# Kernel tuning notes

Hardware: AMD Instinct MI355X
Metric: run time of the kernel (lower is better)

The kernel has to match this reference:

```python
import jax, jax.numpy as jnp
import numpy as np

N, C, T, V = 64, 256, 64, 25

def setup_inputs() -> dict:
    key = jax.random.key(0)
    ks = jax.random.split(key, 11)
    inp = {
        't': jax.random.uniform(ks[0], (1,), dtype=jnp.float32),
        'x': jax.random.normal(ks[1], (N, C, T, V), dtype=jnp.float32),
        'A': jax.random.normal(ks[2], (V, V), dtype=jnp.float32) * 0.2,
    }
    for i in range(4):
        inp[f'w{i+1}'] = jax.random.normal(ks[3 + 2 * i], (C, C), dtype=jnp.float32) * (1.0 / np.sqrt(C))
        inp[f'b{i+1}'] = jax.random.normal(ks[4 + 2 * i], (C,), dtype=jnp.float32) * 0.02
    return inp


def _block(res, A, w, b):
    # graph diffusion over joint dim: A[v,u] @ x[n,c,t,u]
    y = jnp.einsum('vu,nctu->nctv', A, res)
    # 1x1 conv == pointwise channel GEMM
    y = jnp.einsum('oc,nctv->notv', w, y) + b[None, :, None, None]
    return jax.nn.relu(y + res)


def reference(t, x, A, w1, b1, w2, b2, w3, b3, w4, b4):
    # t is unused by the ODE function body (autonomous dynamics)
    res = _block(x, A, w1, b1)
    res = _block(res, A, w2, b2)
    res = _block(res, A, w3, b3)
    res = _block(res, A, w4, b4)
    return res
```

## Files before the change

kernel.cpp:

```cpp
#include <hip/hip_runtime.h>
#include <math.h>

#define NN 64
#define CC 256
#define TT 64
#define VV 25

typedef __bf16 bf16;
typedef __attribute__((ext_vector_type(8)))  __bf16 bf16x8;
typedef __attribute__((ext_vector_type(16))) float  f32x16;
typedef __attribute__((ext_vector_type(4)))  unsigned int uint4v;

#define RS 40

#define OFF_SRES  0
#define OFF_SAB   20480
#define OFF_SBIAS 22528
#define SMEM_BYTES 26624

__global__ void convert_w(const float* __restrict__ w1, const float* __restrict__ w2,
                          const float* __restrict__ w3, const float* __restrict__ w4,
                          bf16* __restrict__ wp) {
    const int gid = blockIdx.x * 256 + threadIdx.x;
    const int e8  = gid * 8;
    const int blk = e8 >> 16;
    const int off = e8 & 65535;
    const int row = off >> 8;
    const int col = off & 255;
    const float* src = (blk == 0) ? w1 : (blk == 1) ? w2 : (blk == 2) ? w3 : w4;
    const float4 f0 = *(const float4*)(src + off);
    const float4 f1 = *(const float4*)(src + off + 4);
    bf16x8 o;
    o[0] = (bf16)f0.x; o[1] = (bf16)f0.y; o[2] = (bf16)f0.z; o[3] = (bf16)f0.w;
    o[4] = (bf16)f1.x; o[5] = (bf16)f1.y; o[6] = (bf16)f1.z; o[7] = (bf16)f1.w;
    const int wv = row >> 6, pair = (row >> 5) & 1, l31 = row & 31;
    const int k = col >> 4, lh = (col >> 3) & 1;
    wp += (((size_t)(blk * 4 + wv) * 16 + k) * 1024) + pair * 512 + (lh * 32 + l31) * 8;
    *(bf16x8*)wp = o;
}

#define MFMA(A, B, C) __builtin_amdgcn_mfma_f32_32x32x16_bf16(A, B, C, 0, 0, 0)

static __device__ __forceinline__ unsigned int pkbf(float a, float b) {
    unsigned short lo = __builtin_bit_cast(unsigned short, (__bf16)a);
    unsigned short hi = __builtin_bit_cast(unsigned short, (__bf16)b);
    return (unsigned int)lo | ((unsigned int)hi << 16);
}

__global__ __launch_bounds__(256, 4) void ode_mfma(
    const float* __restrict__ x, const float* __restrict__ Amat,
    const bf16* __restrict__ wp,
    const float* __restrict__ b1, const float* __restrict__ b2,
    const float* __restrict__ b3, const float* __restrict__ b4,
    float* __restrict__ out)
{
    __shared__ __attribute__((aligned(16))) char smem[SMEM_BYTES];
    bf16*  sres  = (bf16*)(smem + OFF_SRES);
    bf16*  sAb   = (bf16*)(smem + OFF_SAB);
    float* sbias = (float*)(smem + OFF_SBIAS);

    const int t    = blockIdx.x;
    const int n    = blockIdx.y;
    const int tid  = threadIdx.x;
    const int wave = tid >> 6;
    const int lane = tid & 63;
    const int lh   = lane >> 5;
    const int l31  = lane & 31;
    const int o0   = wave * 64;

    bf16x8 wA[4], wB[4];
    {
        const bf16* wb0 = wp + ((size_t)wave * 16) * 1024 + lane * 8;
        #pragma unroll
        for (int q = 0; q < 4; ++q) {
            wA[q] = *(const bf16x8*)(wb0 + q * 1024);
            wB[q] = *(const bf16x8*)(wb0 + q * 1024 + 512);
        }
    }

    sbias[0 * CC + tid] = b1[tid];
    sbias[1 * CC + tid] = b2[tid];
    sbias[2 * CC + tid] = b3[tid];
    sbias[3 * CC + tid] = b4[tid];

    for (int i = tid; i < 32 * 32; i += 256) {
        const int v = i >> 5, u = i & 31;
        sAb[i] = (v < VV && u < VV) ? (bf16)Amat[v * VV + u] : (bf16)0.f;
    }

    {
        const float* xb = x + ((size_t)n * CC * TT + t) * VV;
        for (int i = tid; i < CC * VV; i += 256) {
            const int c = i / VV;
            const int v = i - c * VV;
            sres[c * RS + v] = (bf16)xb[(size_t)c * TT * VV + v];
        }
        #pragma unroll
        for (int u = VV; u < 32; ++u) sres[tid * RS + u] = (bf16)0.f;
    }
    __syncthreads();

    const bf16x8 bfA0 = *(const bf16x8*)&sAb[l31 * 32 + lh * 8];
    const bf16x8 bfA1 = *(const bf16x8*)&sAb[l31 * 32 + 16 + lh * 8];

    for (int blk = 0; blk < 4; ++blk) {
        const bf16* wbase = wp + ((size_t)(blk * 4 + wave) * 16) * 1024 + lane * 8;
        f32x16 acc0 = {}, acc1 = {};

        bf16x8 afA[2], afB[2];
        afA[0] = *(const bf16x8*)&sres[l31 * RS + lh * 8];
        afB[0] = *(const bf16x8*)&sres[l31 * RS + 16 + lh * 8];

        #pragma unroll
        for (int ct = 0; ct < 8; ++ct) {
            const int cur = ct & 1;
            if (ct < 7) {
                afA[cur ^ 1] = *(const bf16x8*)&sres[((ct + 1) * 32 + l31) * RS + lh * 8];
                afB[cur ^ 1] = *(const bf16x8*)&sres[((ct + 1) * 32 + l31) * RS + 16 + lh * 8];
            }
            f32x16 dA = {};
            dA = MFMA(afA[cur], bfA0, dA);
            dA = MFMA(afB[cur], bfA1, dA);

            unsigned int w0 = pkbf(dA[0],  dA[1]),  w1 = pkbf(dA[2],  dA[3]);
            unsigned int w2 = pkbf(dA[4],  dA[5]),  w3 = pkbf(dA[6],  dA[7]);
            unsigned int w4 = pkbf(dA[8],  dA[9]),  w5 = pkbf(dA[10], dA[11]);
            unsigned int w6 = pkbf(dA[12], dA[13]), w7 = pkbf(dA[14], dA[15]);
            asm("v_permlane32_swap_b32 %0, %1" : "+v"(w0), "+v"(w2));
            asm("v_permlane32_swap_b32 %0, %1" : "+v"(w1), "+v"(w3));
            asm("v_permlane32_swap_b32 %0, %1" : "+v"(w4), "+v"(w6));
            asm("v_permlane32_swap_b32 %0, %1" : "+v"(w5), "+v"(w7));
            const bf16x8 y0 = __builtin_bit_cast(bf16x8, (uint4v){w0, w1, w2, w3});
            const bf16x8 y1 = __builtin_bit_cast(bf16x8, (uint4v){w4, w5, w6, w7});

            const int k0 = 2 * ct, k1 = 2 * ct + 1;
            acc0 = MFMA(wA[k0 & 3], y0, acc0);
            acc1 = MFMA(wB[k0 & 3], y0, acc1);
            if (k0 + 4 < 16) {
                wA[k0 & 3] = *(const bf16x8*)(wbase + (k0 + 4) * 1024);
                wB[k0 & 3] = *(const bf16x8*)(wbase + (k0 + 4) * 1024 + 512);
            }
            acc0 = MFMA(wA[k1 & 3], y1, acc0);
            acc1 = MFMA(wB[k1 & 3], y1, acc1);
            if (k1 + 4 < 16) {
                wA[k1 & 3] = *(const bf16x8*)(wbase + (k1 + 4) * 1024);
                wB[k1 & 3] = *(const bf16x8*)(wbase + (k1 + 4) * 1024 + 512);
            }
        }
        __syncthreads();

        if (blk < 3) {
            const bf16* wn = wp + ((size_t)((blk + 1) * 4 + wave) * 16) * 1024 + lane * 8;
            #pragma unroll
            for (int q = 0; q < 4; ++q) {
                wA[q] = *(const bf16x8*)(wn + q * 1024);
                wB[q] = *(const bf16x8*)(wn + q * 1024 + 512);
            }
        }

        const int v = l31;
        #define EPILOGUE(ACC, OT)                                                   \
            _Pragma("unroll")                                                       \
            for (int g = 0; g < 4; ++g) {                                           \
                const int ob = o0 + (OT) * 32 + 8 * g + 4 * lh;                     \
                const float4 bq = *(const float4*)&sbias[blk * CC + ob];            \
                _Pragma("unroll")                                                   \
                for (int r = 0; r < 4; ++r) {                                       \
                    const int o = ob + r;                                           \
                    float val = ACC[4 * g + r] + ((const float*)&bq)[r]             \
                              + (float)sres[o * RS + v];                            \
                    val = fmaxf(val, 0.f);                                          \
                    if (v < VV) {                                                   \
                        if (blk < 3) sres[o * RS + v] = (bf16)val;                  \
                        else out[(((size_t)n * CC + o) * TT + t) * VV + v] = val;   \
                    }                                                               \
                }                                                                   \
            }
        EPILOGUE(acc0, 0)
        EPILOGUE(acc1, 1)
        #undef EPILOGUE
        __syncthreads();
    }
}

extern "C" void kernel_launch(void* const* d_in, const int* in_sizes, int n_in,
                              void* d_out, int out_size, void* d_ws, size_t ws_size,
                              hipStream_t stream) {
    const float* x  = (const float*)d_in[1];
    const float* A  = (const float*)d_in[2];
    const float* w1 = (const float*)d_in[3];
    const float* b1 = (const float*)d_in[4];
    const float* w2 = (const float*)d_in[5];
    const float* b2 = (const float*)d_in[6];
    const float* w3 = (const float*)d_in[7];
    const float* b3 = (const float*)d_in[8];
    const float* w4 = (const float*)d_in[9];
    const float* b4 = (const float*)d_in[10];
    float* out = (float*)d_out;
    bf16* wp = (bf16*)d_ws;

    convert_w<<<128, 256, 0, stream>>>(w1, w2, w3, w4, wp);
    dim3 grid(TT, NN);
    ode_mfma<<<grid, 256, 0, stream>>>(x, A, wp, b1, b2, b3, b4, out);
}
```

Measured before the change: 357.3 us.

## Reorder to channel GEMM then graph diffusion with double-buffered transposed residual

Uses associativity to apply the 256x256 channel GEMM first and the 25x25 graph diffusion afterward, so the diffusion MFMA runs once per output tile rather than once per input-channel tile. The residual is stored transposed (joint-major, padded stride) in two ping-pong shared buffers, which removes one of the two barriers per block. The cost is more shared memory per workgroup, which may lower occupancy, and a different bf16 rounding point for the intermediate values.

```diff
diff --git a/kernel.cpp b/kernel.cpp
--- a/kernel.cpp
+++ b/kernel.cpp
@@ -11,12 +11,13 @@
 typedef __attribute__((ext_vector_type(16))) float  f32x16;
 typedef __attribute__((ext_vector_type(4)))  unsigned int uint4v;
 
-#define RS 40
+#define RST 266
 
-#define OFF_SRES  0
-#define OFF_SAB   20480
-#define OFF_SBIAS 22528
-#define SMEM_BYTES 26624
+#define OFF_S0    0
+#define OFF_S1    17024
+#define OFF_SAB   34048
+#define OFF_SBIAS 36096
+#define SMEM_BYTES 40192
 
 __global__ void convert_w(const float* __restrict__ w1, const float* __restrict__ w2,
                           const float* __restrict__ w3, const float* __restrict__ w4,
@@ -55,7 +56,8 @@
     float* __restrict__ out)
 {
     __shared__ __attribute__((aligned(16))) char smem[SMEM_BYTES];
-    bf16*  sres  = (bf16*)(smem + OFF_SRES);
+    bf16*  s0    = (bf16*)(smem + OFF_S0);
+    bf16*  s1    = (bf16*)(smem + OFF_S1);
     bf16*  sAb   = (bf16*)(smem + OFF_SAB);
     float* sbias = (float*)(smem + OFF_SBIAS);
 
@@ -88,15 +90,19 @@
         sAb[i] = (v < VV && u < VV) ? (bf16)Amat[v * VV + u] : (bf16)0.f;
     }
 
+    for (int i = tid; i < 7 * 256; i += 256) {
+        const int r = 25 + (i >> 8), c = i & 255;
+        s0[r * RST + c] = (bf16)0.f;
+        s1[r * RST + c] = (bf16)0.f;
+    }
+
     {
         const float* xb = x + ((size_t)n * CC * TT + t) * VV;
         for (int i = tid; i < CC * VV; i += 256) {
             const int c = i / VV;
             const int v = i - c * VV;
-            sres[c * RS + v] = (bf16)xb[(size_t)c * TT * VV + v];
+            s0[v * RST + c] = (bf16)xb[(size_t)c * TT * VV + v];
         }
-        #pragma unroll
-        for (int u = VV; u < 32; ++u) sres[tid * RS + u] = (bf16)0.f;
     }
     __syncthreads();
 
@@ -104,50 +110,25 @@
     const bf16x8 bfA1 = *(const bf16x8*)&sAb[l31 * 32 + 16 + lh * 8];
 
     for (int blk = 0; blk < 4; ++blk) {
+        bf16* rd = (blk & 1) ? s1 : s0;
+        bf16* wr = (blk & 1) ? s0 : s1;
         const bf16* wbase = wp + ((size_t)(blk * 4 + wave) * 16) * 1024 + lane * 8;
-        f32x16 acc0 = {}, acc1 = {};
 
-        bf16x8 afA[2], afB[2];
-        afA[0] = *(const bf16x8*)&sres[l31 * RS + lh * 8];
-        afB[0] = *(const bf16x8*)&sres[l31 * RS + 16 + lh * 8];
-
+        f32x16 z0 = {}, z1 = {};
+        bf16x8 af[2];
+        af[0] = *(const bf16x8*)&rd[l31 * RST + lh * 8];
         #pragma unroll
-        for (int ct = 0; ct < 8; ++ct) {
-            const int cur = ct & 1;
-            if (ct < 7) {
-                afA[cur ^ 1] = *(const bf16x8*)&sres[((ct + 1) * 32 + l31) * RS + lh * 8];
-                afB[cur ^ 1] = *(const bf16x8*)&sres[((ct + 1) * 32 + l31) * RS + 16 + lh * 8];
-            }
-            f32x16 dA = {};
-            dA = MFMA(afA[cur], bfA0, dA);
-            dA = MFMA(afB[cur], bfA1, dA);
-
-            unsigned int w0 = pkbf(dA[0],  dA[1]),  w1 = pkbf(dA[2],  dA[3]);
-            unsigned int w2 = pkbf(dA[4],  dA[5]),  w3 = pkbf(dA[6],  dA[7]);
-            unsigned int w4 = pkbf(dA[8],  dA[9]),  w5 = pkbf(dA[10], dA[11]);
-            unsigned int w6 = pkbf(dA[12], dA[13]), w7 = pkbf(dA[14], dA[15]);
-            asm("v_permlane32_swap_b32 %0, %1" : "+v"(w0), "+v"(w2));
-            asm("v_permlane32_swap_b32 %0, %1" : "+v"(w1), "+v"(w3));
-            asm("v_permlane32_swap_b32 %0, %1" : "+v"(w4), "+v"(w6));
-            asm("v_permlane32_swap_b32 %0, %1" : "+v"(w5), "+v"(w7));
-            const bf16x8 y0 = __builtin_bit_cast(bf16x8, (uint4v){w0, w1, w2, w3});
-            const bf16x8 y1 = __builtin_bit_cast(bf16x8, (uint4v){w4, w5, w6, w7});
-
-            const int k0 = 2 * ct, k1 = 2 * ct + 1;
-            acc0 = MFMA(wA[k0 & 3], y0, acc0);
-            acc1 = MFMA(wB[k0 & 3], y0, acc1);
-            if (k0 + 4 < 16) {
-                wA[k0 & 3] = *(const bf16x8*)(wbase + (k0 + 4) * 1024);
-                wB[k0 & 3] = *(const bf16x8*)(wbase + (k0 + 4) * 1024 + 512);
-            }
-            acc0 = MFMA(wA[k1 & 3], y1, acc0);
-            acc1 = MFMA(wB[k1 & 3], y1, acc1);
-            if (k1 + 4 < 16) {
-                wA[k1 & 3] = *(const bf16x8*)(wbase + (k1 + 4) * 1024);
-                wB[k1 & 3] = *(const bf16x8*)(wbase + (k1 + 4) * 1024 + 512);
+        for (int k = 0; k < 16; ++k) {
+            if (k < 15)
+                af[(k + 1) & 1] = *(const bf16x8*)&rd[l31 * RST + (k + 1) * 16 + lh * 8];
+            const bf16x8 a = af[k & 1];
+            z0 = MFMA(a, wA[k & 3], z0);
+            z1 = MFMA(a, wB[k & 3], z1);
+            if (k + 4 < 16) {
+                wA[k & 3] = *(const bf16x8*)(wbase + (k + 4) * 1024);
+                wB[k & 3] = *(const bf16x8*)(wbase + (k + 4) * 1024 + 512);
             }
         }
-        __syncthreads();
 
         if (blk < 3) {
             const bf16* wn = wp + ((size_t)((blk + 1) * 4 + wave) * 16) * 1024 + lane * 8;
@@ -158,28 +139,39 @@
             }
         }
 
-        const int v = l31;
-        #define EPILOGUE(ACC, OT)                                                   \
+        #define FINAL_TILE(ZZ, TL)                                                  \
+        {                                                                           \
+            unsigned int a0 = pkbf(ZZ[0],  ZZ[1]),  a1 = pkbf(ZZ[2],  ZZ[3]);       \
+            unsigned int a2 = pkbf(ZZ[4],  ZZ[5]),  a3 = pkbf(ZZ[6],  ZZ[7]);       \
+            unsigned int a4 = pkbf(ZZ[8],  ZZ[9]),  a5 = pkbf(ZZ[10], ZZ[11]);      \
+            unsigned int a6 = pkbf(ZZ[12], ZZ[13]), a7 = pkbf(ZZ[14], ZZ[15]);      \
+            asm("v_permlane32_swap_b32 %0, %1" : "+v"(a0), "+v"(a2));               \
+            asm("v_permlane32_swap_b32 %0, %1" : "+v"(a1), "+v"(a3));               \
+            asm("v_permlane32_swap_b32 %0, %1" : "+v"(a4), "+v"(a6));               \
+            asm("v_permlane32_swap_b32 %0, %1" : "+v"(a5), "+v"(a7));               \
+            const bf16x8 y0 = __builtin_bit_cast(bf16x8, (uint4v){a0, a1, a2, a3}); \
+            const bf16x8 y1 = __builtin_bit_cast(bf16x8, (uint4v){a4, a5, a6, a7}); \
+            f32x16 d = {};                                                          \
+            d = MFMA(bfA0, y0, d);                                                  \
+            d = MFMA(bfA1, y1, d);                                                  \
+            const int o = o0 + (TL) * 32 + l31;                                     \
+            const float bb = sbias[blk * CC + o];                                   \
             _Pragma("unroll")                                                       \
-            for (int g = 0; g < 4; ++g) {                                           \
-                const int ob = o0 + (OT) * 32 + 8 * g + 4 * lh;                     \
-                const float4 bq = *(const float4*)&sbias[blk * CC + ob];            \
-                _Pragma("unroll")                                                   \
-                for (int r = 0; r < 4; ++r) {                                       \
-                    const int o = ob + r;                                           \
-                    float val = ACC[4 * g + r] + ((const float*)&bq)[r]             \
-                              + (float)sres[o * RS + v];                            \
-                    val = fmaxf(val, 0.f);                                          \
-                    if (v < VV) {                                                   \
-                        if (blk < 3) sres[o * RS + v] = (bf16)val;                  \
-                        else out[(((size_t)n * CC + o) * TT + t) * VV + v] = val;   \
-                    }                                                               \
+            for (int q = 0; q < 16; ++q) {                                          \
+                const int v = (q & 3) + 8 * (q >> 2) + 4 * lh;                      \
+                float val = d[q] + bb + (float)rd[v * RST + o];                     \
+                val = fmaxf(val, 0.f);                                              \
+                if (v < VV) {                                                       \
+                    if (blk < 3) wr[v * RST + o] = (bf16)val;                       \
+                    else out[(((size_t)n * CC + o) * TT + t) * VV + v] = val;       \
                 }                                                                   \
-            }
-        EPILOGUE(acc0, 0)
-        EPILOGUE(acc1, 1)
-        #undef EPILOGUE
-        __syncthreads();
+            }                                                                       \
+        }
+        FINAL_TILE(z0, 0)
+        FINAL_TILE(z1, 1)
+        #undef FINAL_TILE
+
+        if (blk < 3) __syncthreads();
     }
 }
 
```

Measured after the change: 365.0 us. 1.02x slower.
